# Performance work log

Hardware: AMD Instinct MI355X
Metric: run time of the kernel (lower is better)

The kernel has to match this reference:

```python
import jax, jax.numpy as jnp
import numpy as np

B, TXT_T, MEL_T = 32, 256, 400
ENC, N_MEL, PRE = 512, 80, 256
ATT_RNN, DEC_RNN, ATT_DIM = 1024, 1024, 128
N_FILT, KS = 32, 31
PAD = (KS - 1) // 2
NEG = -1e9  # score_mask_value


def setup_inputs() -> dict:
    key = jax.random.key(0)
    ks = jax.random.split(key, 20)
    g = lambda k, s: jax.random.normal(k, s, dtype=jnp.float32) * 0.02
    return {
        'memory': jax.random.normal(ks[0], (B, TXT_T, ENC), dtype=jnp.float32),
        'decoder_inputs': jax.random.normal(ks[1], (B, N_MEL, MEL_T), dtype=jnp.float32),
        'memory_lengths': jax.random.randint(ks[2], (B,), TXT_T // 2, TXT_T + 1),
        'prenet_W1': g(ks[3], (PRE, N_MEL)),
        'prenet_W2': g(ks[4], (PRE, PRE)),
        'att_rnn_Wi': g(ks[5], (4 * ATT_RNN, PRE + ENC)),
        'att_rnn_Wh': g(ks[6], (4 * ATT_RNN, ATT_RNN)),
        'att_rnn_b': jnp.zeros((4 * ATT_RNN,), jnp.float32),
        'loc_conv_W': g(ks[7], (N_FILT, 2, KS)),
        'loc_dense_W': g(ks[8], (ATT_DIM, N_FILT)),
        'query_W': g(ks[9], (ATT_DIM, ATT_RNN)),
        'memory_W': g(ks[10], (ATT_DIM, ENC)),
        'v_W': g(ks[11], (1, ATT_DIM)),
        'dec_rnn_Wi': g(ks[12], (4 * DEC_RNN, ATT_RNN + ENC)),
        'dec_rnn_Wh': g(ks[13], (4 * DEC_RNN, DEC_RNN)),
        'dec_rnn_b': jnp.zeros((4 * DEC_RNN,), jnp.float32),
        'proj_W': g(ks[14], (N_MEL, DEC_RNN + ENC)),
        'proj_b': jnp.zeros((N_MEL,), jnp.float32),
        'gate_W': g(ks[15], (1, DEC_RNN + ENC)),
        'gate_b': jnp.zeros((1,), jnp.float32),
    }


def _lstm_cell(x, h, c, Wi, Wh, b):
    gates = x @ Wi.T + h @ Wh.T + b
    i, f, g, o = jnp.split(gates, 4, axis=-1)  # torch LSTMCell gate order
    c_new = jax.nn.sigmoid(f) * c + jax.nn.sigmoid(i) * jnp.tanh(g)
    h_new = jax.nn.sigmoid(o) * jnp.tanh(c_new)
    return h_new, c_new


def _forward(memory, decoder_inputs, memory_lengths,
             prenet_W1, prenet_W2,
             att_rnn_Wi, att_rnn_Wh, att_rnn_b,
             loc_conv_W, loc_dense_W, query_W, memory_W, v_W,
             dec_rnn_Wi, dec_rnn_Wh, dec_rnn_b,
             proj_W, proj_b, gate_W, gate_b):
    # mask: True where padded
    mask = jnp.arange(TXT_T)[None, :] >= memory_lengths[:, None]          # [B, txt_T]
    processed_memory = jnp.einsum('bte,ae->bta', memory, memory_W)        # [B, txt_T, att_dim]

    # teacher-forced inputs: prepend go-frame, drop last; prenet over all frames
    frames = jnp.transpose(decoder_inputs, (2, 0, 1))                     # [mel_T, B, n_mel]
    frames = jnp.concatenate([jnp.zeros((1, B, N_MEL), frames.dtype), frames[:-1]], axis=0)
    x = jax.nn.relu(frames @ prenet_W1.T)
    x = jax.nn.relu(x @ prenet_W2.T)                                      # [mel_T, B, PRE]

    def step(carry, x_t):
        ah, ac, dh, dc, aw, aw_cum, ctx = carry
        # attention RNN
        ah, ac = _lstm_cell(jnp.concatenate([x_t, ctx], -1), ah, ac,
                            att_rnn_Wi, att_rnn_Wh, att_rnn_b)
        # location-sensitive attention
        aw_cat = jnp.stack([aw, aw_cum], axis=1)                          # [B, 2, txt_T]
        loc = jax.lax.conv_general_dilated(aw_cat, loc_conv_W, (1,), [(PAD, PAD)],
                                           dimension_numbers=('NCH', 'OIH', 'NCH'))  # [B, F, txt_T]
        loc = jnp.einsum('bft,af->bta', loc, loc_dense_W)                 # [B, txt_T, att_dim]
        q = (ah @ query_W.T)[:, None, :]                                  # [B, 1, att_dim]
        e = jnp.einsum('bta,a->bt', jnp.tanh(loc + q + processed_memory), v_W[0])
        e = jnp.where(mask, NEG, e)
        aw_new = jax.nn.softmax(e, axis=1)                                # [B, txt_T]
        ctx = jnp.einsum('bt,bte->be', aw_new, memory)                    # [B, ENC]
        aw_cum = aw_cum + aw_new
        # decoder RNN + projection
        dh, dc = _lstm_cell(jnp.concatenate([ah, ctx], -1), dh, dc,
                            dec_rnn_Wi, dec_rnn_Wh, dec_rnn_b)
        hc = jnp.concatenate([dh, ctx], -1)                               # [B, DEC_RNN+ENC]
        mel = hc @ proj_W.T + proj_b                                      # [B, n_mel]
        gate = (hc @ gate_W.T + gate_b)[:, 0]                             # [B]
        return (ah, ac, dh, dc, aw_new, aw_cum, ctx), (mel, gate, aw_new)

    z = jnp.zeros
    init = (z((B, ATT_RNN)), z((B, ATT_RNN)), z((B, DEC_RNN)), z((B, DEC_RNN)),
            z((B, TXT_T)), z((B, TXT_T)), z((B, ENC)))
    _, (mels, gates, aligns) = jax.lax.scan(step, init, x)
    mel_outputs = jnp.transpose(mels, (1, 2, 0))                          # [B, n_mel, mel_T]
    gate_outputs = jnp.transpose(gates, (1, 0))                           # [B, mel_T]
    alignments = jnp.transpose(aligns, (1, 0, 2))                         # [B, mel_T, txt_T]
    return mel_outputs, gate_outputs, alignments


def reference(memory, decoder_inputs, memory_lengths,
              prenet_W1, prenet_W2,
              att_rnn_Wi, att_rnn_Wh, att_rnn_b,
              loc_conv_W, loc_dense_W, query_W, memory_W, v_W,
              dec_rnn_Wi, dec_rnn_Wh, dec_rnn_b,
              proj_W, proj_b, gate_W, gate_b):
    return _forward(memory, decoder_inputs, memory_lengths,
                    prenet_W1, prenet_W2,
                    att_rnn_Wi, att_rnn_Wh, att_rnn_b,
                    loc_conv_W, loc_dense_W, query_W, memory_W, v_W,
                    dec_rnn_Wi, dec_rnn_Wh, dec_rnn_b,
                    proj_W, proj_b, gate_W, gate_b)
```

## Files before the change

### kernel.cpp

```cpp
#include <hip/hip_runtime.h>
#include <stdint.h>

typedef unsigned short u16;
typedef unsigned long long u64;
typedef __attribute__((ext_vector_type(8))) short short8;
typedef __attribute__((ext_vector_type(4))) float f32x4;

#define NBLK 256
#define NTHR 512
#define LDS_BYTES 158144

__device__ __forceinline__ float bf2f(u16 u){
  union { unsigned int i; float f; } v; v.i = ((unsigned int)u) << 16; return v.f;
}
__device__ __forceinline__ u16 f2bf(float f){
  union { float f; unsigned int i; } v; v.f = f;
  unsigned int u = v.i;
  u += 0x7fffu + ((u >> 16) & 1u);
  return (u16)(u >> 16);
}
__device__ __forceinline__ unsigned int pk2(float a, float b){
  return (unsigned int)f2bf(a) | ((unsigned int)f2bf(b) << 16);
}
__device__ __forceinline__ float sigm(float x){ return 1.f/(1.f + expf(-x)); }

__device__ __forceinline__ u64 coh_ld64(const void* p){
  return __hip_atomic_load((const u64*)p, __ATOMIC_RELAXED, __HIP_MEMORY_SCOPE_AGENT);
}
__device__ __forceinline__ float coh_ldf(const float* p){
  return __hip_atomic_load(p, __ATOMIC_RELAXED, __HIP_MEMORY_SCOPE_AGENT);
}
__device__ __forceinline__ unsigned int coh_ldu(const unsigned int* p){
  return __hip_atomic_load(p, __ATOMIC_RELAXED, __HIP_MEMORY_SCOPE_AGENT);
}
__device__ __forceinline__ void coh_stf(float* p, float v){
  __hip_atomic_store(p, v, __ATOMIC_RELAXED, __HIP_MEMORY_SCOPE_AGENT);
}
__device__ __forceinline__ void coh_stu(unsigned int* p, unsigned int v){
  __hip_atomic_store(p, v, __ATOMIC_RELAXED, __HIP_MEMORY_SCOPE_AGENT);
}
__device__ __forceinline__ void coh_st64(void* p, u64 v){
  __hip_atomic_store((u64*)p, v, __ATOMIC_RELAXED, __HIP_MEMORY_SCOPE_AGENT);
}

struct DP {
  const float *memory, *dec_in, *pW1, *pW2, *aWi, *aWh, *ab;
  const float *cW, *ldW, *qW, *mW, *vW, *dWi, *dWh, *db, *pjW, *pjb, *gW, *gb;
  const int* lens;
  u16 *xfrag, *h1f, *w2f, *wfA, *wfC, *ckf;
  float *pmT, *e_buf, *ah, *dh, *ctx;
  u16 *Xdyn, *Yf;
  float *aw, *awc;
  unsigned int* bar;
  float *out_mel, *out_gate, *out_align;
};

__device__ __forceinline__ int frag_off(int m15, int kk){
  return ((m15) | ((kk >> 3) << 4)) * 8 + (kk & 7);
}

template<int NB>
__device__ __forceinline__ void mfma_ab_batch(const u16* abase0, const u16* wlds, int c0, int l,
                                              f32x4& acc0, f32x4& acc1){
  u64 q0[NB], q1[NB], q2[NB], q3[NB];
  #pragma unroll
  for (int t = 0; t < NB; ++t){
    const u16* ab = abase0 + (size_t)(c0 + t)*1024 + l*8;
    q0[t] = coh_ld64(ab);
    q1[t] = coh_ld64(ab + 4);
    q2[t] = coh_ld64(ab + 512);
    q3[t] = coh_ld64(ab + 516);
  }
  #pragma unroll
  for (int t = 0; t < NB; ++t){
    short8 bfr = *(const short8*)(wlds + ((c0 + t)*64 + l)*8);
    union { u64 q[2]; short8 v; } a0, a1;
    a0.q[0] = q0[t]; a0.q[1] = q1[t];
    a1.q[0] = q2[t]; a1.q[1] = q3[t];
    acc0 = __builtin_amdgcn_mfma_f32_16x16x32_bf16(a0.v, bfr, acc0, 0, 0, 0);
    acc1 = __builtin_amdgcn_mfma_f32_16x16x32_bf16(a1.v, bfr, acc1, 0, 0, 0);
  }
}


__global__ void k_pre1(DP p){
  int t = blockIdx.x >> 5, b = blockIdx.x & 31;
  int tid = threadIdx.x;
  __shared__ float fr[80];
  if (tid < 80) fr[tid] = (t == 0) ? 0.f : p.dec_in[(b*80 + tid)*400 + (t-1)];
  __syncthreads();
  const float* w = p.pW1 + (size_t)tid*80;
  float s = 0.f;
  #pragma unroll
  for (int m4 = 0; m4 < 20; ++m4){
    float4 wv = *(const float4*)(w + m4*4);
    s += wv.x*fr[m4*4] + wv.y*fr[m4*4+1] + wv.z*fr[m4*4+2] + wv.w*fr[m4*4+3];
  }
  s = fmaxf(s, 0.f);
  int row = blockIdx.x;
  int rt = row >> 4, m15 = row & 15;
  int kc = tid >> 5, kk = tid & 31;
  p.h1f[(size_t)(rt*8 + kc)*512 + frag_off(m15, kk)] = f2bf(s);
}

__global__ void k_h2(DP p){
  int rt = blockIdx.x;
  int tid = threadIdx.x, w = tid >> 6, l = tid & 63;
  const u16* abase = p.h1f + (size_t)rt*8*512;
  short8 af[8];
  #pragma unroll
  for (int kc = 0; kc < 8; ++kc) af[kc] = *(const short8*)(abase + kc*512 + l*8);
  for (int nt = w; nt < 16; nt += 4){
    f32x4 acc = {0.f,0.f,0.f,0.f};
    #pragma unroll
    for (int kc = 0; kc < 8; ++kc){
      short8 bf = *(const short8*)(p.w2f + (size_t)((nt*8 + kc)*64 + l)*8);
      acc = __builtin_amdgcn_mfma_f32_16x16x32_bf16(af[kc], bf, acc, 0, 0, 0);
    }
    int ncol = l & 15, rg = l >> 4;
    #pragma unroll
    for (int r = 0; r < 4; ++r){
      float v = fmaxf(acc[r], 0.f);
      int row = rt*16 + rg*4 + r;
      int t = row >> 5, b = row & 31;
      int n = nt*16 + ncol;
      int ch = n >> 5, kk = n & 31, mt = b >> 4;
      p.xfrag[(size_t)((t*8 + ch)*2 + mt)*512 + frag_off(b & 15, kk)] = f2bf(v);
    }
  }
}

__global__ void k_pm(DP p){
  int b = blockIdx.x & 31, tt = blockIdx.x >> 5;
  int tid = threadIdx.x;
  __shared__ u16 ml[32*516];
  for (int s = tid; s < 32*512; s += 512){
    int r = s >> 9, e = s & 511;
    ml[r*516 + e] = f2bf(p.memory[(size_t)((b*256) + tt*32 + r)*512 + e]);
  }
  __syncthreads();
  int a = tid >> 2, tg = tid & 3;
  const float* wr = p.mW + (size_t)a*512;
  float acc[8];
  #pragma unroll
  for (int m = 0; m < 8; ++m) acc[m] = 0.f;
  for (int e8 = 0; e8 < 64; ++e8){
    float4 w0 = *(const float4*)(wr + e8*8);
    float4 w1 = *(const float4*)(wr + e8*8 + 4);
    float wf[8] = {w0.x,w0.y,w0.z,w0.w,w1.x,w1.y,w1.z,w1.w};
    #pragma unroll
    for (int q = 0; q < 8; ++q){
      int e = e8*8 + q;
      #pragma unroll
      for (int m = 0; m < 8; ++m) acc[m] += wf[q] * bf2f(ml[(tg*8 + m)*516 + e]);
    }
  }
  float* dst = p.pmT + (size_t)(b*128 + a)*256 + tt*32 + tg*8;
  f32x4 v0 = {acc[0],acc[1],acc[2],acc[3]}, v1 = {acc[4],acc[5],acc[6],acc[7]};
  *(f32x4*)dst = v0; *(f32x4*)(dst + 4) = v1;
}

__global__ void k_ck(DP p){
  int s = blockIdx.x*512 + threadIdx.x;
  if (s >= 8192) return;
  int slice = s >> 10;
  int rem = s & 1023;
  int l = (rem >> 3) & 63, j = rem & 7, kc = rem >> 9;
  int a = slice*16 + (l & 15), k = kc*32 + ((l >> 4) << 3) + j;
  float val = 0.f;
  if (k != 31 && k != 63){
    int c = (k >= 32) ? 1 : 0, tap = k - (c ? 32 : 0);
    for (int f = 0; f < 32; ++f)
      val += p.ldW[a*32 + f] * p.cW[(f*2 + c)*31 + tap];
  }
  p.ckf[s] = f2bf(val);
}

__global__ void k_wfrag(DP p){
  int g = blockIdx.x*512 + threadIdx.x;
  const int GA = 256*56*64;
  const int GC = 256*80*64;
  const float* src;
  u16* dst;
  if (g < GA){
    int j = g / (56*64); int rem = g - j*56*64; int ch = rem >> 6; int l = rem & 63;
    int c = l & 15, R = ((c >> 2) << 10) + j*4 + (c & 3);
    int k0 = ch*32 + ((l >> 4) << 3);
    src = (k0 < 768) ? (p.aWi + (size_t)R*768 + k0) : (p.aWh + (size_t)R*1024 + (k0 - 768));
    dst = p.wfA + (size_t)g*8;
  } else if (g < GA + GC){
    int g2 = g - GA;
    int j = g2 / (80*64); int rem = g2 - j*80*64; int ch = rem >> 6; int l = rem & 63;
    int c = l & 15, R = ((c >> 2) << 10) + j*4 + (c & 3);
    int k0 = ch*32 + ((l >> 4) << 3);
    src = (k0 < 1536) ? (p.dWi + (size_t)R*1536 + k0) : (p.dWh + (size_t)R*1024 + (k0 - 1536));
    dst = p.wfC + (size_t)g2*8;
  } else {
    int g3 = g - GA - GC;
    int nt = g3 >> 9; int rem = g3 & 511; int kc = rem >> 6; int l = rem & 63;
    src = p.pW2 + (size_t)(nt*16 + (l & 15))*256 + kc*32 + ((l >> 4) << 3);
    dst = p.w2f + (size_t)g3*8;
  }
  float4 v0 = *(const float4*)src;
  float4 v1 = *(const float4*)(src + 4);
  uint4 o;
  o.x = pk2(v0.x, v0.y); o.y = pk2(v0.z, v0.w);
  o.z = pk2(v1.x, v1.y); o.w = pk2(v1.z, v1.w);
  *(uint4*)dst = o;
}

__device__ __forceinline__ void gbar(unsigned int* slots, unsigned int ep){
  __syncthreads();
  if (threadIdx.x == 0){
    coh_stu(&slots[blockIdx.x << 4], ep);
  }
  if (threadIdx.x < 64){
    const int base = threadIdx.x << 2;
    for (;;){
      unsigned int a = coh_ldu(&slots[(base + 0) << 4]);
      unsigned int b = coh_ldu(&slots[(base + 1) << 4]);
      unsigned int c = coh_ldu(&slots[(base + 2) << 4]);
      unsigned int d = coh_ldu(&slots[(base + 3) << 4]);
      bool ok = (a >= ep) & (b >= ep) & (c >= ep) & (d >= ep);
      if (__all(ok)) break;
    }
  }
  asm volatile("" ::: "memory");
  __syncthreads();
}

__launch_bounds__(NTHR, 2)
__global__ void k_decoder(DP p){
  extern __shared__ char smem[];
  u16*   wA     = (u16*)smem;
  u16*   wC     = (u16*)(smem + 57344);
  float* bias_l = (float*)(smem + 139264);
  char*  uni    = smem + 139392;
  float* redA  = (float*)uni;
  float* redC  = (float*)(uni + 8192);
  float* aw_l  = (float*)uni;
  float* q_l   = (float*)(uni + 2304);
  u16*   im2   = (u16*)(uni + 2368);
  float* e_l   = (float*)uni;
  float* r_l   = (float*)(uni + 1024);
  float* awn_l = (float*)(uni + 1088);

  const int blk = blockIdx.x;
  const int tid = threadIdx.x;
  const int bb = blk & 31, rr = blk >> 5;
  const int w = tid >> 6, l = tid & 63;

  {
    const uint4* s  = (const uint4*)(p.wfA + (size_t)blk*56*512);
    uint4* d = (uint4*)wA;
    for (int i2 = tid; i2 < 3584; i2 += NTHR) d[i2] = s[i2];
    const uint4* s2 = (const uint4*)(p.wfC + (size_t)blk*80*512);
    uint4* d2 = (uint4*)wC;
    for (int i2 = tid; i2 < 5120; i2 += NTHR) d2[i2] = s2[i2];
    if (tid < 16){
      int R = ((tid >> 2) << 10) + blk*4 + (tid & 3);
      bias_l[tid] = p.ab[R];
    } else if (tid < 32){
      int c = tid - 16;
      int R = ((c >> 2) << 10) + blk*4 + (c & 3);
      bias_l[tid] = p.db[R];
    }
  }
  __syncthreads();

  float att_c = 0.f, dec_c = 0.f;
  unsigned int ep = 0;

  for (int i = 0; i <= 400; ++i){
    const bool hasA = (i < 400), hasC = (i > 0);

    if (hasA && w < 4){
      f32x4 acc0 = {0.f,0.f,0.f,0.f}, acc1 = {0.f,0.f,0.f,0.f};
      const u16* xd = p.Xdyn + (size_t)(i & 1)*57344;
      int c0 = w*14;
      mfma_ab_batch<7>(xd, wA, c0,     l, acc0, acc1);
      mfma_ab_batch<7>(xd, wA, c0 + 7, l, acc0, acc1);
      int cc = l & 15, rg = l >> 4;
      *(f32x4*)(redA + (((w*2 + 0)*16 + cc) << 4) + (rg << 2)) = acc0;
      *(f32x4*)(redA + (((w*2 + 1)*16 + cc) << 4) + (rg << 2)) = acc1;
    }
    if (hasC && w >= 4){
      f32x4 acc0 = {0.f,0.f,0.f,0.f}, acc1 = {0.f,0.f,0.f,0.f};
      const u16* yb = p.Yf + (size_t)((i + 1) & 1)*81920;
      int c0 = (w - 4)*20;
      mfma_ab_batch<7>(yb, wC, c0,      l, acc0, acc1);
      mfma_ab_batch<7>(yb, wC, c0 + 7,  l, acc0, acc1);
      mfma_ab_batch<6>(yb, wC, c0 + 14, l, acc0, acc1);
      int cc = l & 15, rg = l >> 4, w4 = w - 4;
      *(f32x4*)(redC + (((w4*2 + 0)*16 + cc) << 4) + (rg << 2)) = acc0;
      *(f32x4*)(redC + (((w4*2 + 1)*16 + cc) << 4) + (rg << 2)) = acc1;
    }
    __syncthreads();
    if (hasA && tid < 128){
      int b = tid >> 2, d = tid & 3, mt = b >> 4, b15 = b & 15;
      float gi = bias_l[d], gf = bias_l[4 + d], gg = bias_l[8 + d], go = bias_l[12 + d];
      #pragma unroll
      for (int w2 = 0; w2 < 4; ++w2){
        const float* base = redA + (((w2*2 + mt)*16) << 4) + b15;
        gi += base[(d) << 4]; gf += base[(4 + d) << 4];
        gg += base[(8 + d) << 4]; go += base[(12 + d) << 4];
      }
      att_c = sigm(gf)*att_c + sigm(gi)*tanhf(gg);
      float h = sigm(go)*tanhf(att_c);
      int hidx = blk*4 + d;
      coh_stf(&p.ah[b*1024 + hidx], h);
      unsigned int hv = (unsigned int)f2bf(h);
      unsigned int ov = __shfl_xor(hv, 1, 64);
      if ((d & 1) == 0){
        unsigned int pk = hv | (ov << 16);
        { int k = hidx; int ch = k >> 5, kk = k & 31;
          coh_stu((unsigned int*)&p.Yf[(size_t)(((i & 1)*80 + ch)*2 + mt)*512 + frag_off(b15, kk)], pk); }
        { int k = 768 + hidx; int ch = k >> 5, kk = k & 31;
          coh_stu((unsigned int*)&p.Xdyn[(size_t)((((i + 1) & 1)*56 + ch)*2 + mt)*512 + frag_off(b15, kk)], pk); }
      }
    }
    if (hasC && tid >= 128 && tid < 256){
      int t2 = tid - 128;
      int b = t2 >> 2, d = t2 & 3, mt = b >> 4, b15 = b & 15;
      float gi = bias_l[16 + d], gf = bias_l[16 + 4 + d], gg = bias_l[16 + 8 + d], go = bias_l[16 + 12 + d];
      #pragma unroll
      for (int w2 = 0; w2 < 4; ++w2){
        const float* base = redC + (((w2*2 + mt)*16) << 4) + b15;
        gi += base[(d) << 4]; gf += base[(4 + d) << 4];
        gg += base[(8 + d) << 4]; go += base[(12 + d) << 4];
      }
      dec_c = sigm(gf)*dec_c + sigm(gi)*tanhf(gg);
      float h = sigm(go)*tanhf(dec_c);
      int hidx = blk*4 + d;
      coh_stf(&p.dh[b*1024 + hidx], h);
      unsigned int hv = (unsigned int)f2bf(h);
      unsigned int ov = __shfl_xor(hv, 1, 64);
      if ((d & 1) == 0){
        unsigned int pk = hv | (ov << 16);
        int k = 1536 + hidx; int ch = k >> 5, kk = k & 31;
        coh_stu((unsigned int*)&p.Yf[(size_t)(((i & 1)*80 + ch)*2 + mt)*512 + frag_off(b15, kk)], pk);
      }
    }
    gbar(p.bar, ++ep);

    if (hasA){
      float* sh_f = (float*)im2;
      for (int s = tid; s < 576; s += NTHR){
        int c = s / 288, o = s - c*288;
        float v2 = 0.f;
        if (o >= 16 && o < 272)
          v2 = c ? coh_ldf(&p.awc[bb*256 + (o - 16)]) : coh_ldf(&p.aw[bb*256 + (o - 16)]);
        aw_l[s] = v2;
      }
      sh_f[tid]       = coh_ldf(&p.ah[bb*1024 + tid]);
      sh_f[512 + tid] = coh_ldf(&p.ah[bb*1024 + 512 + tid]);
      __syncthreads();
      {
        int asub = tid >> 5, ksub = tid & 31;
        const float* qwr = p.qW + (size_t)(rr*16 + asub)*1024;
        float s = 0.f;
        for (int m = 0; m < 32; ++m){
          int k = ksub + (m << 5);
          s += qwr[k] * sh_f[k];
        }
        s += __shfl_xor(s, 16, 32); s += __shfl_xor(s, 8, 32);
        s += __shfl_xor(s, 4, 32);  s += __shfl_xor(s, 2, 32); s += __shfl_xor(s, 1, 32);
        if (ksub == 0) q_l[asub] = s;
      }
      __syncthreads();
      #pragma unroll 1
      for (int hh = 0; hh < 2; ++hh){
        for (int s = tid; s < 8192; s += NTHR){
          int jj = s & 7, ll = (s >> 3) & 63, kc = (s >> 9) & 1, mt = s >> 10;
          int trow = hh*128 + mt*16 + (ll & 15);
          int k = kc*32 + ((ll >> 4) << 3) + jj;
          float v2 = 0.f;
          if (k < 31) v2 = aw_l[1 + trow + k];
          else if (k >= 32 && k < 63) v2 = aw_l[289 + trow + (k - 32)];
          im2[s] = f2bf(v2);
        }
        __syncthreads();
        {
          f32x4 acc = {0.f,0.f,0.f,0.f};
          short8 a0 = *(const short8*)(im2 + ((w*2 + 0)*64 + l)*8);
          short8 b0 = *(const short8*)(p.ckf + (size_t)rr*1024 + (0*64 + l)*8);
          short8 a1 = *(const short8*)(im2 + ((w*2 + 1)*64 + l)*8);
          short8 b1 = *(const short8*)(p.ckf + (size_t)rr*1024 + (1*64 + l)*8);
          acc = __builtin_amdgcn_mfma_f32_16x16x32_bf16(a0, b0, acc, 0, 0, 0);
          acc = __builtin_amdgcn_mfma_f32_16x16x32_bf16(a1, b1, acc, 0, 0, 0);
          int a_l = l & 15, rg = l >> 4;
          float q_a = q_l[a_l];
          float va = p.vW[rr*16 + a_l];
          int tbase = hh*128 + w*16 + rg*4;
          const float* pmr = p.pmT + (size_t)(bb*128 + rr*16 + a_l)*256 + tbase;
          f32x4 pv = *(const f32x4*)pmr;
          float e0 = va * tanhf(acc[0] + q_a + pv[0]);
          float e1 = va * tanhf(acc[1] + q_a + pv[1]);
          float e2 = va * tanhf(acc[2] + q_a + pv[2]);
          float e3 = va * tanhf(acc[3] + q_a + pv[3]);
          #pragma unroll
          for (int msk = 8; msk >= 1; msk >>= 1){
            e0 += __shfl_xor(e0, msk, 16);
            e1 += __shfl_xor(e1, msk, 16);
            e2 += __shfl_xor(e2, msk, 16);
            e3 += __shfl_xor(e3, msk, 16);
          }
          if (a_l == 0){
            union { float f[4]; u64 q[2]; } evv;
            evv.f[0]=e0; evv.f[1]=e1; evv.f[2]=e2; evv.f[3]=e3;
            u64* dst = (u64*)(p.e_buf + (size_t)(bb*8 + rr)*256 + tbase);
            coh_st64(&dst[0], evv.q[0]);
            coh_st64(&dst[1], evv.q[1]);
          }
        }
        __syncthreads();
      }
    }
    if (hasC){
      float* sh_f = (float*)im2;
      for (int s = tid; s < 1536; s += NTHR){
        float v = (s < 1024) ? coh_ldf(&p.dh[bb*1024 + s])
                             : coh_ldf(&p.ctx[bb*512 + (s - 1024)]);
        sh_f[s] = v;
      }
      __syncthreads();
      int grp = tid >> 5, gl = tid & 31;
      int cnt = (rr == 7) ? 11 : 10;
      if (grp < cnt){
        int r = rr*10 + grp;
        const float* wrow = (r < 80) ? (p.pjW + (size_t)r*1536) : p.gW;
        float s = 0.f;
        for (int k = gl; k < 1536; k += 32) s += wrow[k] * sh_f[k];
        s += __shfl_xor(s, 16, 32); s += __shfl_xor(s, 8, 32);
        s += __shfl_xor(s, 4, 32);  s += __shfl_xor(s, 2, 32); s += __shfl_xor(s, 1, 32);
        if (gl == 0){
          if (r < 80) p.out_mel[(size_t)(bb*80 + r)*400 + (i - 1)] = s + p.pjb[r];
          else        p.out_gate[bb*400 + (i - 1)] = s + p.gb[0];
        }
      }
    }
    if (i == 400) break;
    gbar(p.bar, ++ep);

    {
      int len = p.lens[bb];
      if (tid < 256){
        float av[8];
        #pragma unroll
        for (int r2 = 0; r2 < 8; ++r2)
          av[r2] = coh_ldf(&p.e_buf[(size_t)(bb*8 + r2)*256 + tid]);
        float s = ((av[0]+av[1])+(av[2]+av[3])) + ((av[4]+av[5])+(av[6]+av[7]));
        if (tid >= len) s = -1e9f;
        e_l[tid] = s;
      }
      if (rr == 1 && bb < 8 && i < 399){
        int idx = (bb << 9) | tid;
        unsigned int val = ((const unsigned int*)(p.xfrag + (size_t)(i + 1)*8192))[idx];
        coh_stu((unsigned int*)(p.Xdyn + (size_t)((i + 1) & 1)*57344) + idx, val);
      }
      __syncthreads();
      float v2 = (tid < 256) ? e_l[tid] : -3.0e38f;
      #pragma unroll
      for (int off = 32; off >= 1; off >>= 1) v2 = fmaxf(v2, __shfl_xor(v2, off, 64));
      if ((tid & 63) == 0) r_l[tid >> 6] = v2;
      __syncthreads();
      if (tid == 0){
        float m2 = r_l[0];
        #pragma unroll
        for (int w2 = 1; w2 < 8; ++w2) m2 = fmaxf(m2, r_l[w2]);
        r_l[8] = m2;
      }
      __syncthreads();
      float mx = r_l[8];
      float exv = (tid < 256) ? expf(e_l[tid] - mx) : 0.f;
      float sv = exv;
      #pragma unroll
      for (int off = 32; off >= 1; off >>= 1) sv += __shfl_xor(sv, off, 64);
      if ((tid & 63) == 0) r_l[tid >> 6] = sv;
      __syncthreads();
      if (tid == 0){
        float ss = 0.f;
        #pragma unroll
        for (int w2 = 0; w2 < 8; ++w2) ss += r_l[w2];
        r_l[9] = 1.f / ss;
      }
      __syncthreads();
      float awn = exv * r_l[9];
      if (tid < 256){
        awn_l[tid] = awn;
        if (rr == 0){
          coh_stf(&p.aw[bb*256 + tid], awn);
          float c0 = coh_ldf(&p.awc[bb*256 + tid]);
          coh_stf(&p.awc[bb*256 + tid], c0 + awn);
          p.out_align[(size_t)(bb*400 + i)*256 + tid] = awn;
        }
      }
      __syncthreads();
      {
        int el = rr*64 + (tid >> 3), g = tid & 7;
        const float* mr = p.memory + (size_t)bb*256*512 + el;
        float s2 = 0.f;
        for (int t2 = g; t2 < 256; t2 += 8) s2 += awn_l[t2] * mr[(size_t)t2*512];
        s2 += __shfl_xor(s2, 4, 8); s2 += __shfl_xor(s2, 2, 8); s2 += __shfl_xor(s2, 1, 8);
        if (g == 0){
          coh_stf(&p.ctx[bb*512 + el], s2);
          unsigned int cv = (unsigned int)f2bf(s2);
          unsigned int ov = __shfl_xor(cv, 8, 64);
          if (((tid >> 3) & 1) == 0){
            unsigned int pk = cv | (ov << 16);
            int mt = bb >> 4, b15 = bb & 15;
            { int k = 1024 + el; int ch = k >> 5, kk = k & 31;
              coh_stu((unsigned int*)&p.Yf[(size_t)(((i & 1)*80 + ch)*2 + mt)*512 + frag_off(b15, kk)], pk); }
            { int k = 256 + el; int ch = k >> 5, kk = k & 31;
              coh_stu((unsigned int*)&p.Xdyn[(size_t)((((i + 1) & 1)*56 + ch)*2 + mt)*512 + frag_off(b15, kk)], pk); }
          }
        }
      }
    }
    gbar(p.bar, ++ep);
  }
}

extern "C" void kernel_launch(void* const* d_in, const int* in_sizes, int n_in,
                              void* d_out, int out_size, void* d_ws, size_t ws_size,
                              hipStream_t stream){
  (void)in_sizes; (void)n_in; (void)out_size; (void)ws_size;
  DP p;
  p.memory = (const float*)d_in[0];
  p.dec_in = (const float*)d_in[1];
  p.lens   = (const int*)d_in[2];
  p.pW1 = (const float*)d_in[3];  p.pW2 = (const float*)d_in[4];
  p.aWi = (const float*)d_in[5];  p.aWh = (const float*)d_in[6];  p.ab = (const float*)d_in[7];
  p.cW  = (const float*)d_in[8];  p.ldW = (const float*)d_in[9];  p.qW = (const float*)d_in[10];
  p.mW  = (const float*)d_in[11]; p.vW  = (const float*)d_in[12];
  p.dWi = (const float*)d_in[13]; p.dWh = (const float*)d_in[14]; p.db = (const float*)d_in[15];
  p.pjW = (const float*)d_in[16]; p.pjb = (const float*)d_in[17];
  p.gW  = (const float*)d_in[18]; p.gb  = (const float*)d_in[19];

  char* ws = (char*)d_ws;
  size_t o = 0;
  auto take = [&](size_t bytes)->char*{ char* r = ws + o; o += (bytes + 255) & ~(size_t)255; return r; };
  p.xfrag = (u16*)take((size_t)3276800*2);
  p.h1f   = (u16*)take((size_t)3276800*2);
  p.w2f   = (u16*)take((size_t)65536*2);
  p.wfA   = (u16*)take((size_t)7340032*2);
  p.wfC   = (u16*)take((size_t)10485760*2);
  p.ckf   = (u16*)take((size_t)8192*2);
  p.pmT   = (float*)take((size_t)1048576*4);
  p.e_buf = (float*)take((size_t)65536*4);
  p.ah    = (float*)take((size_t)32768*4);
  p.dh    = (float*)take((size_t)32768*4);
  p.ctx   = (float*)take((size_t)16384*4);
  char* z0 = ws + o;
  p.Xdyn  = (u16*)take((size_t)114688*2);
  p.Yf    = (u16*)take((size_t)163840*2);
  p.aw    = (float*)take((size_t)8192*4);
  p.awc   = (float*)take((size_t)8192*4);
  p.bar   = (unsigned int*)take(256*64);
  size_t zbytes = (size_t)((ws + o) - z0);

  float* out = (float*)d_out;
  p.out_mel   = out;
  p.out_gate  = out + 1024000;
  p.out_align = out + 1036800;

  hipMemsetAsync(z0, 0, zbytes, stream);
  k_pre1 <<<dim3(12800), dim3(256), 0, stream>>>(p);
  k_wfrag<<<dim3(4368),  dim3(512), 0, stream>>>(p);
  k_ck   <<<dim3(16),    dim3(512), 0, stream>>>(p);
  k_pm   <<<dim3(256),   dim3(512), 0, stream>>>(p);
  k_h2   <<<dim3(800),   dim3(256), 0, stream>>>(p);

  hipFuncSetAttribute(reinterpret_cast<const void*>(k_decoder),
                      hipFuncAttributeMaxDynamicSharedMemorySize, LDS_BYTES);
  DP pp = p;
  void* args[] = { &pp };
  hipError_t err = hipLaunchCooperativeKernel(reinterpret_cast<void*>(k_decoder),
                                              dim3(NBLK), dim3(NTHR), args,
                                              (unsigned int)LDS_BYTES, stream);
  if (err != hipSuccess){
    k_decoder<<<dim3(NBLK), dim3(NTHR), LDS_BYTES, stream>>>(pp);
  }
}
```

Before: 17.49 ms.

## Rebalance LSTM GEMM warps, use fast transcendentals, and trim softmax barriers

```diff
diff --git a/kernel.cpp b/kernel.cpp
--- a/kernel.cpp
+++ b/kernel.cpp
@@ -8,7 +8,7 @@
 
 #define NBLK 256
 #define NTHR 512
-#define LDS_BYTES 158144
+#define LDS_BYTES 162240
 
 __device__ __forceinline__ float bf2f(u16 u){
   union { unsigned int i; float f; } v; v.i = ((unsigned int)u) << 16; return v.f;
@@ -22,7 +22,15 @@
 __device__ __forceinline__ unsigned int pk2(float a, float b){
   return (unsigned int)f2bf(a) | ((unsigned int)f2bf(b) << 16);
 }
-__device__ __forceinline__ float sigm(float x){ return 1.f/(1.f + expf(-x)); }
+__device__ __forceinline__ float fsigm(float x){
+  return __fdividef(1.f, 1.f + __expf(-x));
+}
+__device__ __forceinline__ float ftanh(float x){
+  float ax = fabsf(x);
+  float t = __expf(-2.f*ax);
+  float r = __fdividef(1.f - t, 1.f + t);
+  return copysignf(r, x);
+}
 
 __device__ __forceinline__ u64 coh_ld64(const void* p){
   return __hip_atomic_load((const u64*)p, __ATOMIC_RELAXED, __HIP_MEMORY_SCOPE_AGENT);
@@ -60,12 +68,12 @@
 }
 
 template<int NB>
-__device__ __forceinline__ void mfma_ab_batch(const u16* abase0, const u16* wlds, int c0, int l,
-                                              f32x4& acc0, f32x4& acc1){
+__device__ __forceinline__ void gemm_batch(const u16* abase, const u16* wlds, int c0, int l,
+                                           f32x4& acc0, f32x4& acc1){
   u64 q0[NB], q1[NB], q2[NB], q3[NB];
   #pragma unroll
   for (int t = 0; t < NB; ++t){
-    const u16* ab = abase0 + (size_t)(c0 + t)*1024 + l*8;
+    const u16* ab = abase + (size_t)(c0 + t)*1024 + l*8;
     q0[t] = coh_ld64(ab);
     q1[t] = coh_ld64(ab + 4);
     q2[t] = coh_ld64(ab + 512);
@@ -240,10 +248,10 @@
   float* redC  = (float*)(uni + 8192);
   float* aw_l  = (float*)uni;
   float* q_l   = (float*)(uni + 2304);
-  u16*   im2   = (u16*)(uni + 2368);
-  float* e_l   = (float*)uni;
-  float* r_l   = (float*)(uni + 1024);
-  float* awn_l = (float*)(uni + 1088);
+  float* ah_l  = (float*)(uni + 2368);
+  u16*   im2   = (u16*)(uni + 6464);
+  float* r_l   = (float*)uni;
+  float* awn_l = (float*)(uni + 64);
 
   const int blk = blockIdx.x;
   const int tid = threadIdx.x;
@@ -268,45 +276,62 @@
   }
   __syncthreads();
 
+  const int len = p.lens[bb];
   float att_c = 0.f, dec_c = 0.f;
   unsigned int ep = 0;
 
   for (int i = 0; i <= 400; ++i){
     const bool hasA = (i < 400), hasC = (i > 0);
-
-    if (hasA && w < 4){
+    const u16* xd = p.Xdyn + (size_t)(i & 1)*57344;
+    const u16* yb = p.Yf + (size_t)((i + 1) & 1)*81920;
+    const int cc = l & 15, rg = l >> 4;
+
+    if (hasA && w < 3){
       f32x4 acc0 = {0.f,0.f,0.f,0.f}, acc1 = {0.f,0.f,0.f,0.f};
-      const u16* xd = p.Xdyn + (size_t)(i & 1)*57344;
-      int c0 = w*14;
-      mfma_ab_batch<7>(xd, wA, c0,     l, acc0, acc1);
-      mfma_ab_batch<7>(xd, wA, c0 + 7, l, acc0, acc1);
-      int cc = l & 15, rg = l >> 4;
+      int c0 = w*17;
+      gemm_batch<6>(xd, wA, c0,      l, acc0, acc1);
+      gemm_batch<6>(xd, wA, c0 + 6,  l, acc0, acc1);
+      gemm_batch<5>(xd, wA, c0 + 12, l, acc0, acc1);
       *(f32x4*)(redA + (((w*2 + 0)*16 + cc) << 4) + (rg << 2)) = acc0;
       *(f32x4*)(redA + (((w*2 + 1)*16 + cc) << 4) + (rg << 2)) = acc1;
     }
+    if (w == 3){
+      if (hasA){
+        f32x4 acc0 = {0.f,0.f,0.f,0.f}, acc1 = {0.f,0.f,0.f,0.f};
+        gemm_batch<5>(xd, wA, 51, l, acc0, acc1);
+        *(f32x4*)(redA + (((3*2 + 0)*16 + cc) << 4) + (rg << 2)) = acc0;
+        *(f32x4*)(redA + (((3*2 + 1)*16 + cc) << 4) + (rg << 2)) = acc1;
+      }
+      if (hasC){
+        f32x4 acc0 = {0.f,0.f,0.f,0.f}, acc1 = {0.f,0.f,0.f,0.f};
+        gemm_batch<6>(yb, wC, 0, l, acc0, acc1);
+        gemm_batch<6>(yb, wC, 6, l, acc0, acc1);
+        *(f32x4*)(redC + (((0*2 + 0)*16 + cc) << 4) + (rg << 2)) = acc0;
+        *(f32x4*)(redC + (((0*2 + 1)*16 + cc) << 4) + (rg << 2)) = acc1;
+      }
+    }
     if (hasC && w >= 4){
       f32x4 acc0 = {0.f,0.f,0.f,0.f}, acc1 = {0.f,0.f,0.f,0.f};
-      const u16* yb = p.Yf + (size_t)((i + 1) & 1)*81920;
-      int c0 = (w - 4)*20;
-      mfma_ab_batch<7>(yb, wC, c0,      l, acc0, acc1);
-      mfma_ab_batch<7>(yb, wC, c0 + 7,  l, acc0, acc1);
-      mfma_ab_batch<6>(yb, wC, c0 + 14, l, acc0, acc1);
-      int cc = l & 15, rg = l >> 4, w4 = w - 4;
-      *(f32x4*)(redC + (((w4*2 + 0)*16 + cc) << 4) + (rg << 2)) = acc0;
-      *(f32x4*)(redC + (((w4*2 + 1)*16 + cc) << 4) + (rg << 2)) = acc1;
+      int c0 = 12 + (w - 4)*17;
+      gemm_batch<6>(yb, wC, c0,      l, acc0, acc1);
+      gemm_batch<6>(yb, wC, c0 + 6,  l, acc0, acc1);
+      gemm_batch<5>(yb, wC, c0 + 12, l, acc0, acc1);
+      int slot = w - 3;
+      *(f32x4*)(redC + (((slot*2 + 0)*16 + cc) << 4) + (rg << 2)) = acc0;
+      *(f32x4*)(redC + (((slot*2 + 1)*16 + cc) << 4) + (rg << 2)) = acc1;
     }
     __syncthreads();
     if (hasA && tid < 128){
       int b = tid >> 2, d = tid & 3, mt = b >> 4, b15 = b & 15;
       float gi = bias_l[d], gf = bias_l[4 + d], gg = bias_l[8 + d], go = bias_l[12 + d];
       #pragma unroll
-      for (int w2 = 0; w2 < 4; ++w2){
-        const float* base = redA + (((w2*2 + mt)*16) << 4) + b15;
+      for (int s2 = 0; s2 < 4; ++s2){
+        const float* base = redA + (((s2*2 + mt)*16) << 4) + b15;
         gi += base[(d) << 4]; gf += base[(4 + d) << 4];
         gg += base[(8 + d) << 4]; go += base[(12 + d) << 4];
       }
-      att_c = sigm(gf)*att_c + sigm(gi)*tanhf(gg);
-      float h = sigm(go)*tanhf(att_c);
+      att_c = fsigm(gf)*att_c + fsigm(gi)*ftanh(gg);
+      float h = fsigm(go)*ftanh(att_c);
       int hidx = blk*4 + d;
       coh_stf(&p.ah[b*1024 + hidx], h);
       unsigned int hv = (unsigned int)f2bf(h);
@@ -324,13 +349,13 @@
       int b = t2 >> 2, d = t2 & 3, mt = b >> 4, b15 = b & 15;
       float gi = bias_l[16 + d], gf = bias_l[16 + 4 + d], gg = bias_l[16 + 8 + d], go = bias_l[16 + 12 + d];
       #pragma unroll
-      for (int w2 = 0; w2 < 4; ++w2){
-        const float* base = redC + (((w2*2 + mt)*16) << 4) + b15;
+      for (int s2 = 0; s2 < 5; ++s2){
+        const float* base = redC + (((s2*2 + mt)*16) << 4) + b15;
         gi += base[(d) << 4]; gf += base[(4 + d) << 4];
         gg += base[(8 + d) << 4]; go += base[(12 + d) << 4];
       }
-      dec_c = sigm(gf)*dec_c + sigm(gi)*tanhf(gg);
-      float h = sigm(go)*tanhf(dec_c);
+      dec_c = fsigm(gf)*dec_c + fsigm(gi)*ftanh(gg);
+      float h = fsigm(go)*ftanh(dec_c);
       int hidx = blk*4 + d;
       coh_stf(&p.dh[b*1024 + hidx], h);
       unsigned int hv = (unsigned int)f2bf(h);
@@ -344,7 +369,6 @@
     gbar(p.bar, ++ep);
 
     if (hasA){
-      float* sh_f = (float*)im2;
       for (int s = tid; s < 576; s += NTHR){
         int c = s / 288, o = s - c*288;
         float v2 = 0.f;
@@ -352,34 +376,36 @@
           v2 = c ? coh_ldf(&p.awc[bb*256 + (o - 16)]) : coh_ldf(&p.aw[bb*256 + (o - 16)]);
         aw_l[s] = v2;
       }
-      sh_f[tid]       = coh_ldf(&p.ah[bb*1024 + tid]);
-      sh_f[512 + tid] = coh_ldf(&p.ah[bb*1024 + 512 + tid]);
+      ah_l[tid]       = coh_ldf(&p.ah[bb*1024 + tid]);
+      ah_l[512 + tid] = coh_ldf(&p.ah[bb*1024 + 512 + tid]);
       __syncthreads();
       {
         int asub = tid >> 5, ksub = tid & 31;
         const float* qwr = p.qW + (size_t)(rr*16 + asub)*1024;
         float s = 0.f;
+        #pragma unroll 8
         for (int m = 0; m < 32; ++m){
           int k = ksub + (m << 5);
-          s += qwr[k] * sh_f[k];
+          s += qwr[k] * ah_l[k];
         }
         s += __shfl_xor(s, 16, 32); s += __shfl_xor(s, 8, 32);
         s += __shfl_xor(s, 4, 32);  s += __shfl_xor(s, 2, 32); s += __shfl_xor(s, 1, 32);
         if (ksub == 0) q_l[asub] = s;
       }
       __syncthreads();
-      #pragma unroll 1
       for (int hh = 0; hh < 2; ++hh){
-        for (int s = tid; s < 8192; s += NTHR){
-          int jj = s & 7, ll = (s >> 3) & 63, kc = (s >> 9) & 1, mt = s >> 10;
-          int trow = hh*128 + mt*16 + (ll & 15);
+        #pragma unroll
+        for (int t = 0; t < 16; ++t){
+          int s = (w << 10) + (t << 6) + l;
+          int jj = s & 7, ll = (s >> 3) & 63, kc = (s >> 9) & 1;
+          int trow = hh*128 + w*16 + (ll & 15);
           int k = kc*32 + ((ll >> 4) << 3) + jj;
           float v2 = 0.f;
           if (k < 31) v2 = aw_l[1 + trow + k];
           else if (k >= 32 && k < 63) v2 = aw_l[289 + trow + (k - 32)];
           im2[s] = f2bf(v2);
         }
-        __syncthreads();
+        asm volatile("s_waitcnt lgkmcnt(0)" ::: "memory");
         {
           f32x4 acc = {0.f,0.f,0.f,0.f};
           short8 a0 = *(const short8*)(im2 + ((w*2 + 0)*64 + l)*8);
@@ -388,16 +414,16 @@
           short8 b1 = *(const short8*)(p.ckf + (size_t)rr*1024 + (1*64 + l)*8);
           acc = __builtin_amdgcn_mfma_f32_16x16x32_bf16(a0, b0, acc, 0, 0, 0);
           acc = __builtin_amdgcn_mfma_f32_16x16x32_bf16(a1, b1, acc, 0, 0, 0);
-          int a_l = l & 15, rg = l >> 4;
+          int a_l = l & 15;
           float q_a = q_l[a_l];
           float va = p.vW[rr*16 + a_l];
           int tbase = hh*128 + w*16 + rg*4;
           const float* pmr = p.pmT + (size_t)(bb*128 + rr*16 + a_l)*256 + tbase;
           f32x4 pv = *(const f32x4*)pmr;
-          float e0 = va * tanhf(acc[0] + q_a + pv[0]);
-          float e1 = va * tanhf(acc[1] + q_a + pv[1]);
-          float e2 = va * tanhf(acc[2] + q_a + pv[2]);
-          float e3 = va * tanhf(acc[3] + q_a + pv[3]);
+          float e0 = va * ftanh(acc[0] + q_a + pv[0]);
+          float e1 = va * ftanh(acc[1] + q_a + pv[1]);
+          float e2 = va * ftanh(acc[2] + q_a + pv[2]);
+          float e3 = va * ftanh(acc[3] + q_a + pv[3]);
           #pragma unroll
           for (int msk = 8; msk >= 1; msk >>= 1){
             e0 += __shfl_xor(e0, msk, 16);
@@ -413,10 +439,10 @@
             coh_st64(&dst[1], evv.q[1]);
           }
         }
-        __syncthreads();
       }
     }
     if (hasC){
+      __syncthreads();
       float* sh_f = (float*)im2;
       for (int s = tid; s < 1536; s += NTHR){
         float v = (s < 1024) ? coh_ldf(&p.dh[bb*1024 + s])
@@ -443,15 +469,18 @@
     gbar(p.bar, ++ep);
 
     {
-      int len = p.lens[bb];
+      float s = -3.0e38f, exv = 0.f;
       if (tid < 256){
         float av[8];
         #pragma unroll
         for (int r2 = 0; r2 < 8; ++r2)
           av[r2] = coh_ldf(&p.e_buf[(size_t)(bb*8 + r2)*256 + tid]);
-        float s = ((av[0]+av[1])+(av[2]+av[3])) + ((av[4]+av[5])+(av[6]+av[7]));
+        s = ((av[0]+av[1])+(av[2]+av[3])) + ((av[4]+av[5])+(av[6]+av[7]));
         if (tid >= len) s = -1e9f;
-        e_l[tid] = s;
+        float mv = s;
+        #pragma unroll
+        for (int off = 32; off >= 1; off >>= 1) mv = fmaxf(mv, __shfl_xor(mv, off, 64));
+        if (l == 0) r_l[w] = mv;
       }
       if (rr == 1 && bb < 8 && i < 399){
         int idx = (bb << 9) | tid;
@@ -459,34 +488,18 @@
         coh_stu((unsigned int*)(p.Xdyn + (size_t)((i + 1) & 1)*57344) + idx, val);
       }
       __syncthreads();
-      float v2 = (tid < 256) ? e_l[tid] : -3.0e38f;
-      #pragma unroll
-      for (int off = 32; off >= 1; off >>= 1) v2 = fmaxf(v2, __shfl_xor(v2, off, 64));
-      if ((tid & 63) == 0) r_l[tid >> 6] = v2;
-      __syncthreads();
-      if (tid == 0){
-        float m2 = r_l[0];
+      if (tid < 256){
+        float mx = fmaxf(fmaxf(r_l[0], r_l[1]), fmaxf(r_l[2], r_l[3]));
+        exv = __expf(s - mx);
+        float sv = exv;
         #pragma unroll
-        for (int w2 = 1; w2 < 8; ++w2) m2 = fmaxf(m2, r_l[w2]);
-        r_l[8] = m2;
-      }
-      __syncthreads();
-      float mx = r_l[8];
-      float exv = (tid < 256) ? expf(e_l[tid] - mx) : 0.f;
-      float sv = exv;
-      #pragma unroll
-      for (int off = 32; off >= 1; off >>= 1) sv += __shfl_xor(sv, off, 64);
-      if ((tid & 63) == 0) r_l[tid >> 6] = sv;
-      __syncthreads();
-      if (tid == 0){
-        float ss = 0.f;
-        #pragma unroll
-        for (int w2 = 0; w2 < 8; ++w2) ss += r_l[w2];
-        r_l[9] = 1.f / ss;
-      }
-      __syncthreads();
-      float awn = exv * r_l[9];
+        for (int off = 32; off >= 1; off >>= 1) sv += __shfl_xor(sv, off, 64);
+        if (l == 0) r_l[4 + w] = sv;
+      }
+      __syncthreads();
       if (tid < 256){
+        float tot = (r_l[4] + r_l[5]) + (r_l[6] + r_l[7]);
+        float awn = exv * __fdividef(1.f, tot);
         awn_l[tid] = awn;
         if (rr == 0){
           coh_stf(&p.aw[bb*256 + tid], awn);
```

After: 15.93 ms. -8.9%, faster.
